# Performance work log

Measured on AMD Instinct MI355X. Metric: run time of the kernel, lower is better.

Reference implementation:

```python
import jax, jax.numpy as jnp
import numpy as np

D_MODEL = 1024
NUM_HEADS = 16
D_K = D_MODEL // NUM_HEADS


def setup_inputs() -> dict:
    key = jax.random.key(0)
    ks = jax.random.split(key, 5)
    B, S = 4, 2048
    scale = 1.0 / np.sqrt(D_MODEL)
    x = jax.random.normal(ks[0], (B, S, D_MODEL), dtype=jnp.float32)
    Wq = jax.random.normal(ks[1], (D_MODEL, D_MODEL), dtype=jnp.float32) * scale
    Wk = jax.random.normal(ks[2], (D_MODEL, D_MODEL), dtype=jnp.float32) * scale
    Wv = jax.random.normal(ks[3], (D_MODEL, D_MODEL), dtype=jnp.float32) * scale
    Wo = jax.random.normal(ks[4], (D_MODEL, D_MODEL), dtype=jnp.float32) * scale
    return {"x": x, "Wq": Wq, "Wk": Wk, "Wv": Wv, "Wo": Wo}


def reference(x, Wq, Wk, Wv, Wo):
    B, S, _ = x.shape
    # projections (torch Linear: y = x @ W^T, no bias)
    def proj(W):
        y = jnp.einsum('bsd,ed->bse', x, W)
        # split heads: (b, s, h*dk) -> (b, h, s, dk)
        return y.reshape(B, S, NUM_HEADS, D_K).transpose(0, 2, 1, 3)
    Q, K, V = proj(Wq), proj(Wk), proj(Wv)
    scores = jnp.einsum('bhqd,bhkd->bhqk', Q, K) / np.sqrt(D_K)
    causal = jnp.tril(jnp.ones((S, S), dtype=bool))
    scores = jnp.where(causal, scores, -jnp.inf)
    attn = jax.nn.softmax(scores, axis=-1)
    out = jnp.einsum('bhqk,bhkd->bhqd', attn, V)
    out = out.transpose(0, 2, 1, 3).reshape(B, S, D_MODEL)
    return jnp.einsum('bse,de->bsd', out, Wo)
```

## Files before the change

kernel.cpp:

```cpp
#include <hip/hip_runtime.h>
#include <hip/hip_bf16.h>

typedef __attribute__((ext_vector_type(8))) short short8;
typedef __attribute__((ext_vector_type(4))) float f32x4;

static constexpr int DM = 1024;
static constexpr int NH = 16;
static constexpr int DK = 64;
static constexpr int SL = 2048;
static constexpr int BB = 4;
static constexpr size_t QKV_ELEMS = (size_t)BB * NH * SL * DK;
static constexpr float NEG_BIG = -30000.0f;
static constexpr float SC_LOG2E = 0.125f * 1.44269504088896340736f;

union PackB { __hip_bfloat16 h[8]; uint4 u; };
union Pack4 { __hip_bfloat16 h[4]; uint2 u; };

typedef __attribute__((address_space(1))) unsigned int gu32;
typedef __attribute__((address_space(3))) unsigned int lu32;
__device__ __forceinline__ void async_copy16(const void* g, void* l) {
    __builtin_amdgcn_global_load_lds((gu32*)g, (lu32*)l, 16, 0, 0);
}

__global__ __launch_bounds__(256)
void cvt_all(const float* __restrict__ x,
             const float* __restrict__ wq, const float* __restrict__ wk,
             const float* __restrict__ wv, const float* __restrict__ wo,
             __hip_bfloat16* __restrict__ dst)
{
    const size_t i = (size_t)blockIdx.x * 256 + threadIdx.x;
    const float* src; size_t local;
    if (i < 2097152) { src = x; local = i; }
    else {
        const size_t j = i - 2097152;
        const int r = (int)(j >> 18);
        local = j & 262143;
        src = (r == 0) ? wq : (r == 1) ? wk : (r == 2) ? wv : wo;
    }
    float4 f = reinterpret_cast<const float4*>(src)[local];
    Pack4 p;
    p.h[0] = __float2bfloat16(f.x); p.h[1] = __float2bfloat16(f.y);
    p.h[2] = __float2bfloat16(f.z); p.h[3] = __float2bfloat16(f.w);
    reinterpret_cast<uint2*>(dst)[i] = p.u;
}

__global__ __launch_bounds__(256)
void gemm_qkv(const __hip_bfloat16* __restrict__ A,
              const __hip_bfloat16* __restrict__ W,
              __hip_bfloat16* __restrict__ q_out,
              __hip_bfloat16* __restrict__ k_out,
              __hip_bfloat16* __restrict__ v_out)
{
    __shared__ __hip_bfloat16 As[128 * 64];
    __shared__ __hip_bfloat16 Bs[128 * 64];
    const int tid  = threadIdx.x;
    const int m0   = blockIdx.x * 128;
    const int n0   = blockIdx.y * 128;
    const int w    = tid >> 6;
    const int lane = tid & 63;
    const int quad = lane >> 4;
    const int ln   = lane & 15;
    const int wm   = (w & 1) * 64;
    const int wn   = (w >> 1) * 64;
    const int srow = lane >> 3;
    const int sch  = ((lane & 7) ^ srow) * 8;

    f32x4 acc[4][4] = {};

    for (int k0 = 0; k0 < DM; k0 += 64) {
        #pragma unroll
        for (int j = 0; j < 4; j++) {
            const int rbase = w * 32 + j * 8;
            async_copy16(A + (size_t)(m0 + rbase + srow) * DM + k0 + sch,
                         &As[rbase * 64]);
            async_copy16(W + (size_t)(n0 + rbase + srow) * DM + k0 + sch,
                         &Bs[rbase * 64]);
        }
        __syncthreads();

        #pragma unroll
        for (int ks = 0; ks < 2; ks++) {
            short8 a[4], b[4];
            #pragma unroll
            for (int i = 0; i < 4; i++)
                a[i] = *reinterpret_cast<const short8*>(
                    &As[(wm + i*16 + ln) * 64 + (((ks*4 + quad) ^ (ln & 7)) * 8)]);
            #pragma unroll
            for (int j = 0; j < 4; j++)
                b[j] = *reinterpret_cast<const short8*>(
                    &Bs[(wn + j*16 + ln) * 64 + (((ks*4 + quad) ^ (ln & 7)) * 8)]);
            #pragma unroll
            for (int i = 0; i < 4; i++)
                #pragma unroll
                for (int j = 0; j < 4; j++)
                    acc[i][j] = __builtin_amdgcn_mfma_f32_16x16x32_bf16(a[i], b[j], acc[i][j], 0, 0, 0);
        }
        __syncthreads();
    }

    #pragma unroll
    for (int i = 0; i < 4; i++) {
        #pragma unroll
        for (int j = 0; j < 4; j++) {
            #pragma unroll
            for (int r = 0; r < 4; r++) {
                const int m = m0 + wm + i*16 + quad*4 + r;
                const int n = n0 + wn + j*16 + ln;
                const int b_ = m >> 11;
                const int s  = m & 2047;
                const int which = n >> 10;
                const int nn = n & 1023;
                const int h  = nn >> 6;
                const int d  = nn & 63;
                const __hip_bfloat16 v = __float2bfloat16(acc[i][j][r]);
                if (which == 0)
                    q_out[((size_t)((b_*NH + h)*SL + s))*DK + d] = v;
                else if (which == 1)
                    k_out[((size_t)((b_*NH + h)*SL + s))*DK + d] = v;
                else
                    v_out[((size_t)((b_*NH + h)*DK + d))*SL + s] = v;
            }
        }
    }
}

__global__ __launch_bounds__(256)
void gemm_wo(const __hip_bfloat16* __restrict__ A,
             const __hip_bfloat16* __restrict__ W,
             float* __restrict__ outp)
{
    __shared__ __hip_bfloat16 As[128 * 64];
    __shared__ __hip_bfloat16 Bs[128 * 64];
    const int tid  = threadIdx.x;
    const int m0   = blockIdx.x * 128;
    const int n0   = blockIdx.y * 128;
    const int w    = tid >> 6;
    const int lane = tid & 63;
    const int quad = lane >> 4;
    const int ln   = lane & 15;
    const int wm   = (w & 1) * 64;
    const int wn   = (w >> 1) * 64;
    const int srow = lane >> 3;
    const int sch  = ((lane & 7) ^ srow) * 8;

    f32x4 acc[4][4] = {};

    for (int k0 = 0; k0 < DM; k0 += 64) {
        #pragma unroll
        for (int j = 0; j < 4; j++) {
            const int rbase = w * 32 + j * 8;
            async_copy16(A + (size_t)(m0 + rbase + srow) * DM + k0 + sch,
                         &As[rbase * 64]);
            async_copy16(W + (size_t)(n0 + rbase + srow) * DM + k0 + sch,
                         &Bs[rbase * 64]);
        }
        __syncthreads();

        #pragma unroll
        for (int ks = 0; ks < 2; ks++) {
            short8 a[4], b[4];
            #pragma unroll
            for (int i = 0; i < 4; i++)
                a[i] = *reinterpret_cast<const short8*>(
                    &As[(wm + i*16 + ln) * 64 + (((ks*4 + quad) ^ (ln & 7)) * 8)]);
            #pragma unroll
            for (int j = 0; j < 4; j++)
                b[j] = *reinterpret_cast<const short8*>(
                    &Bs[(wn + j*16 + ln) * 64 + (((ks*4 + quad) ^ (ln & 7)) * 8)]);
            #pragma unroll
            for (int i = 0; i < 4; i++)
                #pragma unroll
                for (int j = 0; j < 4; j++)
                    acc[i][j] = __builtin_amdgcn_mfma_f32_16x16x32_bf16(a[i], b[j], acc[i][j], 0, 0, 0);
        }
        __syncthreads();
    }

    #pragma unroll
    for (int i = 0; i < 4; i++)
        #pragma unroll
        for (int j = 0; j < 4; j++)
            #pragma unroll
            for (int r = 0; r < 4; r++) {
                const int m = m0 + wm + i*16 + quad*4 + r;
                const int n = n0 + wn + j*16 + ln;
                outp[(size_t)m * DM + n] = acc[i][j][r];
            }
}

template<bool A_BF16, int MODE>
__global__ __launch_bounds__(256)
void gemm_bt(const void* __restrict__ Ap,
             const float* __restrict__ W,
             void* __restrict__ outp)
{
    __shared__ __hip_bfloat16 As[128][40];
    __shared__ __hip_bfloat16 Bs[128][40];
    const int tid  = threadIdx.x;
    const int m0   = blockIdx.x * 128;
    const int n0   = blockIdx.y * 128;
    const int w    = tid >> 6;
    const int lane = tid & 63;
    const int quad = lane >> 4;
    const int ln   = lane & 15;
    const int wm   = (w & 1) * 64;
    const int wn   = (w >> 1) * 64;
    const int lr   = tid >> 1;
    const int lc   = (tid & 1) * 16;

    f32x4 acc[4][4] = {};

    for (int k0 = 0; k0 < DM; k0 += 32) {
        if (A_BF16) {
            const uint4* ap = reinterpret_cast<const uint4*>(
                (const __hip_bfloat16*)Ap + (size_t)(m0 + lr) * DM + k0 + lc);
            uint4 a0 = ap[0], a1 = ap[1];
            *reinterpret_cast<uint4*>(&As[lr][lc])     = a0;
            *reinterpret_cast<uint4*>(&As[lr][lc + 8]) = a1;
        } else {
            const float4* ap = reinterpret_cast<const float4*>(
                (const float*)Ap + (size_t)(m0 + lr) * DM + k0 + lc);
            float4 f0 = ap[0], f1 = ap[1], f2 = ap[2], f3 = ap[3];
            PackB p0, p1;
            p0.h[0] = __float2bfloat16(f0.x); p0.h[1] = __float2bfloat16(f0.y);
            p0.h[2] = __float2bfloat16(f0.z); p0.h[3] = __float2bfloat16(f0.w);
            p0.h[4] = __float2bfloat16(f1.x); p0.h[5] = __float2bfloat16(f1.y);
            p0.h[6] = __float2bfloat16(f1.z); p0.h[7] = __float2bfloat16(f1.w);
            p1.h[0] = __float2bfloat16(f2.x); p1.h[1] = __float2bfloat16(f2.y);
            p1.h[2] = __float2bfloat16(f2.z); p1.h[3] = __float2bfloat16(f2.w);
            p1.h[4] = __float2bfloat16(f3.x); p1.h[5] = __float2bfloat16(f3.y);
            p1.h[6] = __float2bfloat16(f3.z); p1.h[7] = __float2bfloat16(f3.w);
            *reinterpret_cast<uint4*>(&As[lr][lc])     = p0.u;
            *reinterpret_cast<uint4*>(&As[lr][lc + 8]) = p1.u;
        }
        {
            const float4* wp = reinterpret_cast<const float4*>(
                W + (size_t)(n0 + lr) * DM + k0 + lc);
            float4 f0 = wp[0], f1 = wp[1], f2 = wp[2], f3 = wp[3];
            PackB p0, p1;
            p0.h[0] = __float2bfloat16(f0.x); p0.h[1] = __float2bfloat16(f0.y);
            p0.h[2] = __float2bfloat16(f0.z); p0.h[3] = __float2bfloat16(f0.w);
            p0.h[4] = __float2bfloat16(f1.x); p0.h[5] = __float2bfloat16(f1.y);
            p0.h[6] = __float2bfloat16(f1.z); p0.h[7] = __float2bfloat16(f1.w);
            p1.h[0] = __float2bfloat16(f2.x); p1.h[1] = __float2bfloat16(f2.y);
            p1.h[2] = __float2bfloat16(f2.z); p1.h[3] = __float2bfloat16(f2.w);
            p1.h[4] = __float2bfloat16(f3.x); p1.h[5] = __float2bfloat16(f3.y);
            p1.h[6] = __float2bfloat16(f3.z); p1.h[7] = __float2bfloat16(f3.w);
            *reinterpret_cast<uint4*>(&Bs[lr][lc])     = p0.u;
            *reinterpret_cast<uint4*>(&Bs[lr][lc + 8]) = p1.u;
        }
        __syncthreads();

        short8 a[4], b[4];
        #pragma unroll
        for (int i = 0; i < 4; i++)
            a[i] = *reinterpret_cast<const short8*>(&As[wm + i*16 + ln][quad*8]);
        #pragma unroll
        for (int j = 0; j < 4; j++)
            b[j] = *reinterpret_cast<const short8*>(&Bs[wn + j*16 + ln][quad*8]);
        #pragma unroll
        for (int i = 0; i < 4; i++)
            #pragma unroll
            for (int j = 0; j < 4; j++)
                acc[i][j] = __builtin_amdgcn_mfma_f32_16x16x32_bf16(a[i], b[j], acc[i][j], 0, 0, 0);
        __syncthreads();
    }

    #pragma unroll
    for (int i = 0; i < 4; i++) {
        #pragma unroll
        for (int j = 0; j < 4; j++) {
            #pragma unroll
            for (int r = 0; r < 4; r++) {
                const int m = m0 + wm + i*16 + quad*4 + r;
                const int n = n0 + wn + j*16 + ln;
                const float v = acc[i][j][r];
                if (MODE == 2) {
                    ((float*)outp)[(size_t)m * DM + n] = v;
                } else {
                    const int b_ = m >> 11;
                    const int s  = m & 2047;
                    const int h  = n >> 6;
                    const int d  = n & 63;
                    size_t idx;
                    if (MODE == 0) idx = ((size_t)((b_*NH + h)*SL + s))*DK + d;
                    else           idx = ((size_t)((b_*NH + h)*DK + d))*SL + s;
                    ((__hip_bfloat16*)outp)[idx] = __float2bfloat16(v);
                }
            }
        }
    }
}

__global__ __launch_bounds__(256)
void attn_causal(const __hip_bfloat16* __restrict__ Q,
                 const __hip_bfloat16* __restrict__ K,
                 const __hip_bfloat16* __restrict__ Vt,
                 __hip_bfloat16* __restrict__ O)
{
    __shared__ __hip_bfloat16 Ks[64][72];
    __shared__ __hip_bfloat16 Vs[64][72];
    __shared__ __hip_bfloat16 p_lds[4][16][72];

    const int tid  = threadIdx.x;
    const int w    = tid >> 6;
    const int lane = tid & 63;
    const int quad = lane >> 4;
    const int ln   = lane & 15;
    const int bh   = blockIdx.y;
    const int b_   = bh >> 4;
    const int h    = bh & 15;

    const int srow   = tid >> 3;
    const int schunk = (tid & 7) * 8;

    const __hip_bfloat16* Qb = Q  + (size_t)bh * SL * DK;
    const __hip_bfloat16* Kb = K  + (size_t)bh * SL * DK;
    const __hip_bfloat16* Vb = Vt + (size_t)bh * DK * SL;

    for (int pass = 0; pass < 2; ++pass) {
        const int qt    = (pass == 0) ? (int)blockIdx.x : 31 - (int)blockIdx.x;
        const int q0    = qt * 64;
        const int qbase = q0 + w * 16;

        short8 aq0 = *reinterpret_cast<const short8*>(Qb + (size_t)(qbase + ln) * DK + quad*8);
        short8 aq1 = *reinterpret_cast<const short8*>(Qb + (size_t)(qbase + ln) * DK + 32 + quad*8);

        f32x4 acc[4] = {};
        float lsum[4] = {0.f, 0.f, 0.f, 0.f};

        const __hip_bfloat16* Kg = Kb + (size_t)srow * DK + schunk;
        const __hip_bfloat16* Vg = Vb + (size_t)srow * SL + schunk;
        uint4 kv0 = *reinterpret_cast<const uint4*>(Kg);
        uint4 kv1 = *reinterpret_cast<const uint4*>(Kg + 32 * DK);
        uint4 vv0 = *reinterpret_cast<const uint4*>(Vg);
        uint4 vv1 = *reinterpret_cast<const uint4*>(Vg + 32 * SL);

        for (int k0 = 0; k0 <= q0; k0 += 64) {
            __syncthreads();
            *reinterpret_cast<uint4*>(&Ks[srow     ][schunk]) = kv0;
            *reinterpret_cast<uint4*>(&Ks[srow + 32][schunk]) = kv1;
            *reinterpret_cast<uint4*>(&Vs[srow     ][schunk]) = vv0;
            *reinterpret_cast<uint4*>(&Vs[srow + 32][schunk]) = vv1;
            __syncthreads();

            if (k0 + 64 <= q0) {
                const __hip_bfloat16* Kg2 = Kb + (size_t)(k0 + 64 + srow) * DK + schunk;
                const __hip_bfloat16* Vg2 = Vb + (size_t)srow * SL + (k0 + 64) + schunk;
                kv0 = *reinterpret_cast<const uint4*>(Kg2);
                kv1 = *reinterpret_cast<const uint4*>(Kg2 + 32 * DK);
                vv0 = *reinterpret_cast<const uint4*>(Vg2);
                vv1 = *reinterpret_cast<const uint4*>(Vg2 + 32 * SL);
            }

            f32x4 s[4];
            __builtin_amdgcn_s_setprio(1);
            #pragma unroll
            for (int kc = 0; kc < 4; kc++) {
                short8 bk0 = *reinterpret_cast<const short8*>(&Ks[kc*16 + ln][quad*8]);
                short8 bk1 = *reinterpret_cast<const short8*>(&Ks[kc*16 + ln][32 + quad*8]);
                f32x4 z = {};
                z = __builtin_amdgcn_mfma_f32_16x16x32_bf16(aq0, bk0, z, 0, 0, 0);
                z = __builtin_amdgcn_mfma_f32_16x16x32_bf16(aq1, bk1, z, 0, 0, 0);
                s[kc] = z;
            }
            __builtin_amdgcn_s_setprio(0);
            const bool diag = (k0 == q0);
            #pragma unroll
            for (int kc = 0; kc < 4; kc++) {
                #pragma unroll
                for (int r = 0; r < 4; r++) {
                    float v = s[kc][r] * SC_LOG2E;
                    if (diag) {
                        const int kg = k0 + kc*16 + ln;
                        const int qg = qbase + quad*4 + r;
                        if (kg > qg) v = NEG_BIG;
                    }
                    const float p = __builtin_amdgcn_exp2f(v);
                    lsum[r] += p;
                    p_lds[w][quad*4 + r][kc*16 + ln] = __float2bfloat16(p);
                }
            }
            short8 ap0 = *reinterpret_cast<const short8*>(&p_lds[w][ln][quad*8]);
            short8 ap1 = *reinterpret_cast<const short8*>(&p_lds[w][ln][32 + quad*8]);
            __builtin_amdgcn_s_setprio(1);
            #pragma unroll
            for (int nt = 0; nt < 4; nt++) {
                short8 bv0 = *reinterpret_cast<const short8*>(&Vs[nt*16 + ln][quad*8]);
                short8 bv1 = *reinterpret_cast<const short8*>(&Vs[nt*16 + ln][32 + quad*8]);
                acc[nt] = __builtin_amdgcn_mfma_f32_16x16x32_bf16(ap0, bv0, acc[nt], 0, 0, 0);
                acc[nt] = __builtin_amdgcn_mfma_f32_16x16x32_bf16(ap1, bv1, acc[nt], 0, 0, 0);
            }
            __builtin_amdgcn_s_setprio(0);
        }

        #pragma unroll
        for (int r = 0; r < 4; r++) {
            float v = lsum[r];
            v += __shfl_xor(v, 1, 64);
            v += __shfl_xor(v, 2, 64);
            v += __shfl_xor(v, 4, 64);
            v += __shfl_xor(v, 8, 64);
            lsum[r] = v;
        }

        #pragma unroll
        for (int nt = 0; nt < 4; nt++) {
            #pragma unroll
            for (int r = 0; r < 4; r++) {
                const int sI = qbase + quad*4 + r;
                const int d  = nt*16 + ln;
                const float v = acc[nt][r] / lsum[r];
                O[(((size_t)b_ * SL + sI) * NH + h) * DK + d] = __float2bfloat16(v);
            }
        }
    }
}

extern "C" void kernel_launch(void* const* d_in, const int* in_sizes, int n_in,
                              void* d_out, int out_size, void* d_ws, size_t ws_size,
                              hipStream_t stream)
{
    const float* x  = (const float*)d_in[0];
    const float* Wq = (const float*)d_in[1];
    const float* Wk = (const float*)d_in[2];
    const float* Wv = (const float*)d_in[3];
    const float* Wo = (const float*)d_in[4];

    __hip_bfloat16* q_ws = (__hip_bfloat16*)d_ws;
    __hip_bfloat16* k_ws = q_ws + QKV_ELEMS;
    __hip_bfloat16* v_ws = k_ws + QKV_ELEMS;

    const dim3 gb(256);
    const size_t FAST_WS = (3 * QKV_ELEMS + QKV_ELEMS + 4 * (size_t)DM * DM)
                           * sizeof(__hip_bfloat16);

    if (ws_size >= FAST_WS) {
        __hip_bfloat16* xb  = v_ws + QKV_ELEMS;
        __hip_bfloat16* wqb = xb  + QKV_ELEMS;
        __hip_bfloat16* wob = wqb + 3 * (size_t)DM * DM;

        cvt_all<<<12288, 256, 0, stream>>>(x, Wq, Wk, Wv, Wo, xb);

        gemm_qkv<<<dim3(64, 24), gb, 0, stream>>>(xb, wqb, q_ws, k_ws, v_ws);

        attn_causal<<<dim3(16, BB*NH), 256, 0, stream>>>(q_ws, k_ws, v_ws, xb);

        gemm_wo<<<dim3(64, 8), gb, 0, stream>>>(xb, wob, (float*)d_out);
    } else {
        __hip_bfloat16* obuf = (__hip_bfloat16*)d_out;
        float*          fbuf = (float*)d_ws;
        const dim3 gg(64, 8);
        gemm_bt<false, 0><<<gg, gb, 0, stream>>>(x, Wq, q_ws);
        gemm_bt<false, 0><<<gg, gb, 0, stream>>>(x, Wk, k_ws);
        gemm_bt<false, 1><<<gg, gb, 0, stream>>>(x, Wv, v_ws);
        attn_causal<<<dim3(16, BB*NH), 256, 0, stream>>>(q_ws, k_ws, v_ws, obuf);
        gemm_bt<true, 2><<<gg, gb, 0, stream>>>(obuf, Wo, fbuf);
        (void)hipMemcpyAsync(d_out, fbuf, QKV_ELEMS * sizeof(float),
                             hipMemcpyDeviceToDevice, stream);
    }
}
```

Measured before the change: 296.1 us.

## Rewrite causal attention with 32x32 MFMA, register-resident P, and 128-row query tiles

The attention kernel now uses 32x32x16 bf16 MFMAs and computes S^T so each lane owns one query row. The probability tile is packed to bf16 with v_cvt_pk_bf16 and rearranged with v_permlane32_swap, so it feeds the PV MFMA directly instead of round-tripping through LDS. Query tiles grow to 128 rows (32 per wave) with half the grid. Waves whose rows lie entirely above a key tile skip its compute, and row sums reduce with a single shuffle. Output stores are packed. The exchange is more registers per wave and fewer blocks, which can reduce occupancy and hurt load balance.

```diff
diff --git a/kernel.cpp b/kernel.cpp
--- a/kernel.cpp
+++ b/kernel.cpp
@@ -3,6 +3,7 @@
 
 typedef __attribute__((ext_vector_type(8))) short short8;
 typedef __attribute__((ext_vector_type(4))) float f32x4;
+typedef __attribute__((ext_vector_type(16))) float f32x16;
 
 static constexpr int DM = 1024;
 static constexpr int NH = 16;
@@ -20,6 +21,15 @@
 typedef __attribute__((address_space(3))) unsigned int lu32;
 __device__ __forceinline__ void async_copy16(const void* g, void* l) {
     __builtin_amdgcn_global_load_lds((gu32*)g, (lu32*)l, 16, 0, 0);
+}
+
+__device__ __forceinline__ unsigned cvt_pk_bf16(float lo, float hi) {
+    unsigned r;
+    asm("v_cvt_pk_bf16_f32 %0, %1, %2" : "=v"(r) : "v"(lo), "v"(hi));
+    return r;
+}
+__device__ __forceinline__ void pl32_swap(unsigned &a, unsigned &b) {
+    asm("v_permlane32_swap_b32 %0, %1" : "+v"(a), "+v"(b));
 }
 
 __global__ __launch_bounds__(256)
@@ -300,119 +310,138 @@
 {
     __shared__ __hip_bfloat16 Ks[64][72];
     __shared__ __hip_bfloat16 Vs[64][72];
-    __shared__ __hip_bfloat16 p_lds[4][16][72];
 
     const int tid  = threadIdx.x;
     const int w    = tid >> 6;
     const int lane = tid & 63;
-    const int quad = lane >> 4;
-    const int ln   = lane & 15;
+    const int ln32 = lane & 31;
+    const int hi   = lane >> 5;
     const int bh   = blockIdx.y;
     const int b_   = bh >> 4;
     const int h    = bh & 15;
 
-    const int srow   = tid >> 3;
-    const int schunk = (tid & 7) * 8;
+    const int sr = tid >> 3;
+    const int sc = (tid & 7) * 8;
 
     const __hip_bfloat16* Qb = Q  + (size_t)bh * SL * DK;
     const __hip_bfloat16* Kb = K  + (size_t)bh * SL * DK;
     const __hip_bfloat16* Vb = Vt + (size_t)bh * DK * SL;
 
     for (int pass = 0; pass < 2; ++pass) {
-        const int qt    = (pass == 0) ? (int)blockIdx.x : 31 - (int)blockIdx.x;
-        const int q0    = qt * 64;
-        const int qbase = q0 + w * 16;
-
-        short8 aq0 = *reinterpret_cast<const short8*>(Qb + (size_t)(qbase + ln) * DK + quad*8);
-        short8 aq1 = *reinterpret_cast<const short8*>(Qb + (size_t)(qbase + ln) * DK + 32 + quad*8);
-
-        f32x4 acc[4] = {};
-        float lsum[4] = {0.f, 0.f, 0.f, 0.f};
-
-        const __hip_bfloat16* Kg = Kb + (size_t)srow * DK + schunk;
-        const __hip_bfloat16* Vg = Vb + (size_t)srow * SL + schunk;
-        uint4 kv0 = *reinterpret_cast<const uint4*>(Kg);
-        uint4 kv1 = *reinterpret_cast<const uint4*>(Kg + 32 * DK);
-        uint4 vv0 = *reinterpret_cast<const uint4*>(Vg);
-        uint4 vv1 = *reinterpret_cast<const uint4*>(Vg + 32 * SL);
-
-        for (int k0 = 0; k0 <= q0; k0 += 64) {
+        const int qt    = (pass == 0) ? (int)blockIdx.x : 15 - (int)blockIdx.x;
+        const int q0    = qt * 128;
+        const int qbase = q0 + w * 32;
+        const int qg    = qbase + ln32;
+
+        short8 qf[4];
+        #pragma unroll
+        for (int dt = 0; dt < 4; dt++)
+            qf[dt] = *reinterpret_cast<const short8*>(
+                Qb + (size_t)qg * DK + dt*16 + hi*8);
+
+        f32x16 o0 = {}, o1 = {};
+        float lsum = 0.f;
+
+        const int nkt = 2*qt + 2;
+
+        uint4 kr0 = *reinterpret_cast<const uint4*>(Kb + (size_t)sr * DK + sc);
+        uint4 kr1 = *reinterpret_cast<const uint4*>(Kb + (size_t)(32 + sr) * DK + sc);
+        uint4 vr0 = *reinterpret_cast<const uint4*>(Vb + (size_t)sr * SL + sc);
+        uint4 vr1 = *reinterpret_cast<const uint4*>(Vb + (size_t)(32 + sr) * SL + sc);
+
+        for (int it = 0; it < nkt; ++it) {
+            const int k0 = it * 64;
             __syncthreads();
-            *reinterpret_cast<uint4*>(&Ks[srow     ][schunk]) = kv0;
-            *reinterpret_cast<uint4*>(&Ks[srow + 32][schunk]) = kv1;
-            *reinterpret_cast<uint4*>(&Vs[srow     ][schunk]) = vv0;
-            *reinterpret_cast<uint4*>(&Vs[srow + 32][schunk]) = vv1;
+            *reinterpret_cast<uint4*>(&Ks[sr     ][sc]) = kr0;
+            *reinterpret_cast<uint4*>(&Ks[sr + 32][sc]) = kr1;
+            *reinterpret_cast<uint4*>(&Vs[sr     ][sc]) = vr0;
+            *reinterpret_cast<uint4*>(&Vs[sr + 32][sc]) = vr1;
             __syncthreads();
-
-            if (k0 + 64 <= q0) {
-                const __hip_bfloat16* Kg2 = Kb + (size_t)(k0 + 64 + srow) * DK + schunk;
-                const __hip_bfloat16* Vg2 = Vb + (size_t)srow * SL + (k0 + 64) + schunk;
-                kv0 = *reinterpret_cast<const uint4*>(Kg2);
-                kv1 = *reinterpret_cast<const uint4*>(Kg2 + 32 * DK);
-                vv0 = *reinterpret_cast<const uint4*>(Vg2);
-                vv1 = *reinterpret_cast<const uint4*>(Vg2 + 32 * SL);
-            }
-
-            f32x4 s[4];
+            if (it + 1 < nkt) {
+                const int kn = k0 + 64;
+                kr0 = *reinterpret_cast<const uint4*>(Kb + (size_t)(kn + sr) * DK + sc);
+                kr1 = *reinterpret_cast<const uint4*>(Kb + (size_t)(kn + 32 + sr) * DK + sc);
+                vr0 = *reinterpret_cast<const uint4*>(Vb + (size_t)sr * SL + kn + sc);
+                vr1 = *reinterpret_cast<const uint4*>(Vb + (size_t)(32 + sr) * SL + kn + sc);
+            }
+            if (k0 > qbase + 31) continue;
+
+            f32x16 s0 = {}, s1 = {};
             __builtin_amdgcn_s_setprio(1);
             #pragma unroll
-            for (int kc = 0; kc < 4; kc++) {
-                short8 bk0 = *reinterpret_cast<const short8*>(&Ks[kc*16 + ln][quad*8]);
-                short8 bk1 = *reinterpret_cast<const short8*>(&Ks[kc*16 + ln][32 + quad*8]);
-                f32x4 z = {};
-                z = __builtin_amdgcn_mfma_f32_16x16x32_bf16(aq0, bk0, z, 0, 0, 0);
-                z = __builtin_amdgcn_mfma_f32_16x16x32_bf16(aq1, bk1, z, 0, 0, 0);
-                s[kc] = z;
+            for (int dt = 0; dt < 4; dt++) {
+                short8 kf0 = *reinterpret_cast<const short8*>(&Ks[ln32     ][dt*16 + hi*8]);
+                short8 kf1 = *reinterpret_cast<const short8*>(&Ks[32 + ln32][dt*16 + hi*8]);
+                s0 = __builtin_amdgcn_mfma_f32_32x32x16_bf16(kf0, qf[dt], s0, 0, 0, 0);
+                s1 = __builtin_amdgcn_mfma_f32_32x32x16_bf16(kf1, qf[dt], s1, 0, 0, 0);
             }
             __builtin_amdgcn_s_setprio(0);
-            const bool diag = (k0 == q0);
-            #pragma unroll
-            for (int kc = 0; kc < 4; kc++) {
+
+            const bool dodiag = (k0 + 63 > qbase);
+            if (dodiag) {
                 #pragma unroll
-                for (int r = 0; r < 4; r++) {
-                    float v = s[kc][r] * SC_LOG2E;
-                    if (diag) {
-                        const int kg = k0 + kc*16 + ln;
-                        const int qg = qbase + quad*4 + r;
-                        if (kg > qg) v = NEG_BIG;
-                    }
-                    const float p = __builtin_amdgcn_exp2f(v);
-                    lsum[r] += p;
-                    p_lds[w][quad*4 + r][kc*16 + ln] = __float2bfloat16(p);
+                for (int r = 0; r < 16; r++) {
+                    const int km = (r & 3) + 8*(r >> 2) + 4*hi;
+                    float v0 = s0[r] * SC_LOG2E;
+                    float v1 = s1[r] * SC_LOG2E;
+                    if (k0 + km      > qg) v0 = NEG_BIG;
+                    if (k0 + 32 + km > qg) v1 = NEG_BIG;
+                    const float p0 = __builtin_amdgcn_exp2f(v0);
+                    const float p1 = __builtin_amdgcn_exp2f(v1);
+                    s0[r] = p0; s1[r] = p1;
+                    lsum += p0 + p1;
                 }
-            }
-            short8 ap0 = *reinterpret_cast<const short8*>(&p_lds[w][ln][quad*8]);
-            short8 ap1 = *reinterpret_cast<const short8*>(&p_lds[w][ln][32 + quad*8]);
+            } else {
+                #pragma unroll
+                for (int r = 0; r < 16; r++) {
+                    const float p0 = __builtin_amdgcn_exp2f(s0[r] * SC_LOG2E);
+                    const float p1 = __builtin_amdgcn_exp2f(s1[r] * SC_LOG2E);
+                    s0[r] = p0; s1[r] = p1;
+                    lsum += p0 + p1;
+                }
+            }
+
             __builtin_amdgcn_s_setprio(1);
             #pragma unroll
-            for (int nt = 0; nt < 4; nt++) {
-                short8 bv0 = *reinterpret_cast<const short8*>(&Vs[nt*16 + ln][quad*8]);
-                short8 bv1 = *reinterpret_cast<const short8*>(&Vs[nt*16 + ln][32 + quad*8]);
-                acc[nt] = __builtin_amdgcn_mfma_f32_16x16x32_bf16(ap0, bv0, acc[nt], 0, 0, 0);
-                acc[nt] = __builtin_amdgcn_mfma_f32_16x16x32_bf16(ap1, bv1, acc[nt], 0, 0, 0);
+            for (int c = 0; c < 4; c++) {
+                const int R = 8 * (c & 1);
+                unsigned x0, x1, y0, y1;
+                if (c < 2) {
+                    x0 = cvt_pk_bf16(s0[R+0], s0[R+1]);
+                    x1 = cvt_pk_bf16(s0[R+2], s0[R+3]);
+                    y0 = cvt_pk_bf16(s0[R+4], s0[R+5]);
+                    y1 = cvt_pk_bf16(s0[R+6], s0[R+7]);
+                } else {
+                    x0 = cvt_pk_bf16(s1[R+0], s1[R+1]);
+                    x1 = cvt_pk_bf16(s1[R+2], s1[R+3]);
+                    y0 = cvt_pk_bf16(s1[R+4], s1[R+5]);
+                    y1 = cvt_pk_bf16(s1[R+6], s1[R+7]);
+                }
+                pl32_swap(x0, y0);
+                pl32_swap(x1, y1);
+                union { unsigned u[4]; short8 s8; } pf;
+                pf.u[0] = x0; pf.u[1] = x1; pf.u[2] = y0; pf.u[3] = y1;
+                short8 vf0 = *reinterpret_cast<const short8*>(&Vs[ln32     ][c*16 + hi*8]);
+                short8 vf1 = *reinterpret_cast<const short8*>(&Vs[32 + ln32][c*16 + hi*8]);
+                o0 = __builtin_amdgcn_mfma_f32_32x32x16_bf16(vf0, pf.s8, o0, 0, 0, 0);
+                o1 = __builtin_amdgcn_mfma_f32_32x32x16_bf16(vf1, pf.s8, o1, 0, 0, 0);
             }
             __builtin_amdgcn_s_setprio(0);
         }
 
-        #pragma unroll
-        for (int r = 0; r < 4; r++) {
-            float v = lsum[r];
-            v += __shfl_xor(v, 1, 64);
-            v += __shfl_xor(v, 2, 64);
-            v += __shfl_xor(v, 4, 64);
-            v += __shfl_xor(v, 8, 64);
-            lsum[r] = v;
-        }
-
-        #pragma unroll
-        for (int nt = 0; nt < 4; nt++) {
-            #pragma unroll
-            for (int r = 0; r < 4; r++) {
-                const int sI = qbase + quad*4 + r;
-                const int d  = nt*16 + ln;
-                const float v = acc[nt][r] / lsum[r];
-                O[(((size_t)b_ * SL + sI) * NH + h) * DK + d] = __float2bfloat16(v);
-            }
+        const float ls = lsum + __shfl_xor(lsum, 32, 64);
+        const float rq = 1.0f / ls;
+
+        __hip_bfloat16* Orow = O + (((size_t)b_ * SL + qg) * NH + h) * DK;
+        #pragma unroll
+        for (int g = 0; g < 4; g++) {
+            uint2 pk0, pk1;
+            pk0.x = cvt_pk_bf16(o0[4*g+0]*rq, o0[4*g+1]*rq);
+            pk0.y = cvt_pk_bf16(o0[4*g+2]*rq, o0[4*g+3]*rq);
+            pk1.x = cvt_pk_bf16(o1[4*g+0]*rq, o1[4*g+1]*rq);
+            pk1.y = cvt_pk_bf16(o1[4*g+2]*rq, o1[4*g+3]*rq);
+            *reinterpret_cast<uint2*>(Orow + 8*g + 4*hi)      = pk0;
+            *reinterpret_cast<uint2*>(Orow + 32 + 8*g + 4*hi) = pk1;
         }
     }
 }
@@ -444,7 +473,7 @@
 
         gemm_qkv<<<dim3(64, 24), gb, 0, stream>>>(xb, wqb, q_ws, k_ws, v_ws);
 
-        attn_causal<<<dim3(16, BB*NH), 256, 0, stream>>>(q_ws, k_ws, v_ws, xb);
+        attn_causal<<<dim3(8, BB*NH), 256, 0, stream>>>(q_ws, k_ws, v_ws, xb);
 
         gemm_wo<<<dim3(64, 8), gb, 0, stream>>>(xb, wob, (float*)d_out);
     } else {
@@ -454,7 +483,7 @@
         gemm_bt<false, 0><<<gg, gb, 0, stream>>>(x, Wq, q_ws);
         gemm_bt<false, 0><<<gg, gb, 0, stream>>>(x, Wk, k_ws);
         gemm_bt<false, 1><<<gg, gb, 0, stream>>>(x, Wv, v_ws);
-        attn_causal<<<dim3(16, BB*NH), 256, 0, stream>>>(q_ws, k_ws, v_ws, obuf);
+        attn_causal<<<dim3(8, BB*NH), 256, 0, stream>>>(q_ws, k_ws, v_ws, obuf);
         gemm_bt<true, 2><<<gg, gb, 0, stream>>>(obuf, Wo, fbuf);
         (void)hipMemcpyAsync(d_out, fbuf, QKV_ELEMS * sizeof(float),
                              hipMemcpyDeviceToDevice, stream);
```

Result: faster. 256.3 us (-13.5%).
